# Kernel tuning notes

Hardware: AMD Instinct MI355X
Metric: run time of the kernel (lower is better)

Reference implementation:

```python
import jax, jax.numpy as jnp
import numpy as np
import math

B, N, DS, DP, DH, H, PQK, PV = 1, 384, 384, 128, 16, 12, 4, 8
PKV = PQK + PV
EPS = 1e-8
SOFTPLUS_INV_1 = 0.541324854612918


def setup_inputs() -> dict:
    key = jax.random.key(0)
    ks = jax.random.split(key, 20)
    W = lambda k, shp: (jax.random.normal(k, shp, dtype=jnp.float32) * 0.02)
    s = jax.random.normal(ks[0], (B, N, DS), dtype=jnp.float32)
    z = jax.random.normal(ks[1], (B, N, N, DP), dtype=jnp.float32)
    # random rigid frames: orthonormal rotations via QR + translations
    rot = jnp.linalg.qr(jax.random.normal(ks[2], (B, N, 3, 3), dtype=jnp.float32))[0]
    trans = jax.random.normal(ks[3], (B, N, 3), dtype=jnp.float32)
    square_mask = jnp.zeros((B, 1, N, N), dtype=jnp.float32)
    HC = H * DH
    COUT = H * (DP + DH + PV * 4)  # 2112
    return {
        "s": s, "z": z, "rot": rot, "trans": trans, "square_mask": square_mask,
        "Wq": W(ks[4], (DS, HC)), "bq": jnp.zeros((HC,), jnp.float32),
        "Wkv": W(ks[5], (DS, 2 * HC)), "bkv": jnp.zeros((2 * HC,), jnp.float32),
        "Wq_pts": W(ks[6], (DS, H * PQK * 3)), "bq_pts": jnp.zeros((H * PQK * 3,), jnp.float32),
        "Wkv_pts": W(ks[7], (DS, H * PKV * 3)), "bkv_pts": jnp.zeros((H * PKV * 3,), jnp.float32),
        "Wb": W(ks[8], (DP, H)), "bb": jnp.zeros((H,), jnp.float32),
        "head_weights": jnp.full((H,), SOFTPLUS_INV_1, dtype=jnp.float32),
        "Wout": W(ks[9], (COUT, DS)), "bout": jnp.zeros((DS,), jnp.float32),
    }


def _points(lin, rot, trans, npts):
    # lin: [B,N,3*H*npts] laid out as 3 coord-chunks of H*npts each (torch split+stack)
    pts = jnp.swapaxes(lin.reshape(B, N, 3, H * npts), -1, -2)  # [B,N,H*npts,3]
    pts = jnp.einsum('bnij,bnpj->bnpi', rot, pts) + trans[:, :, None, :]  # frame apply
    return pts.reshape(B, N, H, npts, 3)


def reference(s, z, rot, trans, square_mask, Wq, bq, Wkv, bkv, Wq_pts, bq_pts,
              Wkv_pts, bkv_pts, Wb, bb, head_weights, Wout, bout):
    q = (s @ Wq + bq).reshape(B, N, H, DH)
    kv = (s @ Wkv + bkv).reshape(B, N, H, 2 * DH)
    k, v = kv[..., :DH], kv[..., DH:]

    q_pts = _points(s @ Wq_pts + bq_pts, rot, trans, PQK)          # [B,N,H,PQK,3]
    kv_pts = _points(s @ Wkv_pts + bkv_pts, rot, trans, PKV)       # [B,N,H,PKV,3]
    k_pts, v_pts = kv_pts[..., :PQK, :], kv_pts[..., PQK:, :]

    bias = z @ Wb + bb                                             # [B,Nq,Nk,H]
    attn = jnp.einsum('bqhd,bkhd->bhqk', q, k) * math.sqrt(1.0 / (3 * DH))
    attn = attn + math.sqrt(1.0 / 3) * jnp.transpose(bias, (0, 3, 1, 2))

    diff = q_pts[:, :, None] - k_pts[:, None]                      # [B,Nq,Nk,H,PQK,3]
    dist2 = jnp.sum(diff * diff, axis=-1)                          # [B,Nq,Nk,H,PQK]
    hw = jax.nn.softplus(head_weights) * math.sqrt(1.0 / (3 * (PQK * 9.0 / 2)))
    pt_att = -0.5 * jnp.sum(dist2 * hw[None, None, None, :, None], axis=-1)  # [B,Nq,Nk,H]

    attn = attn + square_mask + jnp.transpose(pt_att, (0, 3, 1, 2))
    attn = jax.nn.softmax(attn, axis=-1)                           # [B,H,Nq,Nk]

    o = jnp.einsum('bhqk,bkhd->bqhd', attn, v).reshape(B, N, H * DH)
    o_pts = jnp.einsum('bhqk,bkhpc->bqhpc', attn, v_pts)           # [B,N,H,PV,3]
    # frame invert_apply: R^T (p - t)
    o_pts = jnp.einsum('bnji,bnhpj->bnhpi', rot, o_pts - trans[:, :, None, None, :])
    o_pts_norm = jnp.sqrt(jnp.sum(o_pts ** 2, axis=-1) + EPS).reshape(B, N, H * PV)
    o_pts_flat = o_pts.reshape(B, N, H * PV, 3)
    o_pair = jnp.einsum('bhqk,bqkc->bqhc', attn, z).reshape(B, N, H * DP)

    cat = jnp.concatenate(
        [o, o_pts_flat[..., 0], o_pts_flat[..., 1], o_pts_flat[..., 2], o_pts_norm, o_pair],
        axis=-1)
    return cat @ Wout + bout
```

## Files before the change

kernel.cpp:

```cpp
#include <hip/hip_runtime.h>
#include <math.h>

#define N     384
#define DSd   384
#define DP    128
#define DH    16
#define H     12
#define PQK   4
#define PV    8
#define HC    (H*DH)
#define PROJW 1152
#define NN    (N*N)
#define COUTD 2112
#define KSPL  4
#define KCH   96

__global__ __launch_bounds__(256) void pack_w(
    const float* __restrict__ Wq, const float* __restrict__ Wkv,
    const float* __restrict__ Wqp, const float* __restrict__ Wkvp,
    const float* __restrict__ bq, const float* __restrict__ bkv,
    const float* __restrict__ bqp, const float* __restrict__ bkvp,
    float* __restrict__ Wcat, float* __restrict__ bcat)
{
    const int i = blockIdx.x * 256 + threadIdx.x;
    if (i < DSd * PROJW) {
        const int r = i / PROJW, c = i % PROJW;
        float v;
        if (c < 192)      v = Wq[r*192 + c];
        else if (c < 576) v = Wkv[r*384 + (c-192)];
        else if (c < 720) v = Wqp[r*144 + (c-576)];
        else              v = Wkvp[r*432 + (c-720)];
        Wcat[i] = v;
    }
    if (i < PROJW) {
        float v;
        if (i < 192)      v = bq[i];
        else if (i < 576) v = bkv[i-192];
        else if (i < 720) v = bqp[i-576];
        else              v = bkvp[i-720];
        bcat[i] = v;
    }
}

__global__ __launch_bounds__(256) void gemm32x64(
    const float* __restrict__ A, const float* __restrict__ B,
    float* __restrict__ partial, int M, int Nc, int K, int kchunk)
{
    __shared__ float Ast[32][34];
    __shared__ float Bs[32][68];
    const int tid = threadIdx.x;
    const int tc = tid & 15, tr = tid >> 4;
    const int row0 = blockIdx.x * 32, col0 = blockIdx.y * 64;
    const int kbeg = blockIdx.z * kchunk;
    const int kend = kbeg + kchunk;
    float acc[2][4] = {};

    for (int kk = kbeg; kk < kend; kk += 32) {
        #pragma unroll
        for (int i = tid; i < 32*32; i += 256) {
            int r = i >> 5, c = i & 31;
            Ast[c][r] = A[(row0 + r) * K + kk + c];
        }
        #pragma unroll
        for (int i = tid; i < 32*64; i += 256) {
            int r = i >> 6, c = i & 63;
            Bs[r][c] = B[(kk + r) * Nc + col0 + c];
        }
        __syncthreads();
        #pragma unroll
        for (int p = 0; p < 32; ++p) {
            const float2 av = *(const float2*)&Ast[p][tr*2];
            const float4 bv = *(const float4*)&Bs[p][tc*4];
            acc[0][0] = fmaf(av.x, bv.x, acc[0][0]);
            acc[0][1] = fmaf(av.x, bv.y, acc[0][1]);
            acc[0][2] = fmaf(av.x, bv.z, acc[0][2]);
            acc[0][3] = fmaf(av.x, bv.w, acc[0][3]);
            acc[1][0] = fmaf(av.y, bv.x, acc[1][0]);
            acc[1][1] = fmaf(av.y, bv.y, acc[1][1]);
            acc[1][2] = fmaf(av.y, bv.z, acc[1][2]);
            acc[1][3] = fmaf(av.y, bv.w, acc[1][3]);
        }
        __syncthreads();
    }
    float* p0 = partial + ((size_t)blockIdx.z * M + row0 + tr*2) * Nc + col0 + tc*4;
    *(float4*)p0        = make_float4(acc[0][0], acc[0][1], acc[0][2], acc[0][3]);
    *(float4*)(p0 + Nc) = make_float4(acc[1][0], acc[1][1], acc[1][2], acc[1][3]);
}

__global__ __launch_bounds__(256) void reduce_kernel(
    const float* __restrict__ partial, const float* __restrict__ bias,
    float* __restrict__ out, int nc, int parts, int stride)
{
    const int i = blockIdx.x * 256 + threadIdx.x;
    float a = bias[i % nc];
    for (int t = 0; t < parts; ++t) a += partial[(size_t)t * stride + i];
    out[i] = a;
}

__global__ __launch_bounds__(192) void repack_kernel(
    const float* __restrict__ proj, const float* __restrict__ rot,
    const float* __restrict__ trans,
    float* __restrict__ q_t, float* __restrict__ k_t, float* __restrict__ vcat,
    float* __restrict__ qpts_t, float* __restrict__ kpts_t)
{
    const int n = blockIdx.x;
    const int tid = threadIdx.x;
    const float* pr = proj + n * PROJW;

    {
        int h = tid >> 4, d = tid & 15;
        q_t[(h*N + n)*DH + d]     = pr[h*DH + d];
        k_t[(h*N + n)*DH + d]     = pr[HC + h*2*DH + d];
        vcat[(h*40 + d)*N + n]    = pr[HC + h*2*DH + DH + d];
    }
    const float r00 = rot[n*9+0], r01 = rot[n*9+1], r02 = rot[n*9+2];
    const float r10 = rot[n*9+3], r11 = rot[n*9+4], r12 = rot[n*9+5];
    const float r20 = rot[n*9+6], r21 = rot[n*9+7], r22 = rot[n*9+8];
    const float t0 = trans[n*3+0], t1 = trans[n*3+1], t2 = trans[n*3+2];

    if (tid < H*PQK) {
        int p = tid;
        float l0 = pr[576 + 0*48 + p];
        float l1 = pr[576 + 1*48 + p];
        float l2 = pr[576 + 2*48 + p];
        int h = p / PQK, pt = p % PQK;
        float* dst = qpts_t + (h*N + n)*12 + pt*3;
        dst[0] = r00*l0 + r01*l1 + r02*l2 + t0;
        dst[1] = r10*l0 + r11*l1 + r12*l2 + t1;
        dst[2] = r20*l0 + r21*l1 + r22*l2 + t2;
    }
    if (tid < H*(PQK+PV)) {
        int p = tid;
        float l0 = pr[720 + 0*144 + p];
        float l1 = pr[720 + 1*144 + p];
        float l2 = pr[720 + 2*144 + p];
        int h = p / 12, pt = p % 12;
        float x0 = r00*l0 + r01*l1 + r02*l2 + t0;
        float x1 = r10*l0 + r11*l1 + r12*l2 + t1;
        float x2 = r20*l0 + r21*l1 + r22*l2 + t2;
        if (pt < PQK) {
            float* dst = kpts_t + (h*N + n)*12 + pt*3;
            dst[0] = x0; dst[1] = x1; dst[2] = x2;
        } else {
            const int j = 16 + (pt - PQK)*3;
            vcat[(h*40 + j+0)*N + n] = x0;
            vcat[(h*40 + j+1)*N + n] = x1;
            vcat[(h*40 + j+2)*N + n] = x2;
        }
    }
}

__global__ __launch_bounds__(256) void bias_kernel(
    const float* __restrict__ z, const float* __restrict__ Wb,
    const float* __restrict__ bb, float* __restrict__ biasattn)
{
    const int pair = blockIdx.x * 256 + threadIdx.x;
    const float4* zp = (const float4*)(z + (size_t)pair * DP);
    float acc[12] = {};
    #pragma unroll 4
    for (int c4 = 0; c4 < DP/4; ++c4) {
        const float4 zv = zp[c4];
        #pragma unroll
        for (int h = 0; h < H; ++h) {
            acc[h] = fmaf(zv.x, Wb[(c4*4+0)*H + h], acc[h]);
            acc[h] = fmaf(zv.y, Wb[(c4*4+1)*H + h], acc[h]);
            acc[h] = fmaf(zv.z, Wb[(c4*4+2)*H + h], acc[h]);
            acc[h] = fmaf(zv.w, Wb[(c4*4+3)*H + h], acc[h]);
        }
    }
    const float sc = 0.5773502691896258f;
    #pragma unroll
    for (int h = 0; h < H; ++h)
        biasattn[h*NN + pair] = (acc[h] + bb[h]) * sc;
}

__global__ __launch_bounds__(128) void attn_kernel(
    const float* __restrict__ q_t, const float* __restrict__ k_t,
    const float* __restrict__ qpts_t, const float* __restrict__ kpts_t,
    const float* __restrict__ mask, const float* __restrict__ head_weights,
    float* __restrict__ biasattn)
{
    const int h  = blockIdx.x % H;
    const int qi = blockIdx.x / H;
    const int tid = threadIdx.x;
    __shared__ float logits[N];
    __shared__ float red[4];

    const float4* qv = (const float4*)(q_t + (h*N + qi)*DH);
    const float4 q0 = qv[0], q1 = qv[1], q2 = qv[2], q3 = qv[3];
    const float4* qpv = (const float4*)(qpts_t + (h*N + qi)*12);
    const float4 p0 = qpv[0], p1 = qpv[1], p2 = qpv[2];
    const float hw = log1pf(expf(head_weights[h])) * 0.13608276348795434f;

    float lmax = -1e30f;
    for (int k = tid; k < N; k += 128) {
        const float4* kr = (const float4*)(k_t + (h*N + k)*DH);
        const float4 a0 = kr[0], a1 = kr[1], a2 = kr[2], a3 = kr[3];
        float dot = q0.x*a0.x;
        dot = fmaf(q0.y, a0.y, dot); dot = fmaf(q0.z, a0.z, dot); dot = fmaf(q0.w, a0.w, dot);
        dot = fmaf(q1.x, a1.x, dot); dot = fmaf(q1.y, a1.y, dot); dot = fmaf(q1.z, a1.z, dot); dot = fmaf(q1.w, a1.w, dot);
        dot = fmaf(q2.x, a2.x, dot); dot = fmaf(q2.y, a2.y, dot); dot = fmaf(q2.z, a2.z, dot); dot = fmaf(q2.w, a2.w, dot);
        dot = fmaf(q3.x, a3.x, dot); dot = fmaf(q3.y, a3.y, dot); dot = fmaf(q3.z, a3.z, dot); dot = fmaf(q3.w, a3.w, dot);
        const float4* kp = (const float4*)(kpts_t + (h*N + k)*12);
        const float4 b0 = kp[0], b1 = kp[1], b2 = kp[2];
        float df, d2;
        df = p0.x-b0.x; d2 = df*df;
        df = p0.y-b0.y; d2 = fmaf(df, df, d2);
        df = p0.z-b0.z; d2 = fmaf(df, df, d2);
        df = p0.w-b0.w; d2 = fmaf(df, df, d2);
        df = p1.x-b1.x; d2 = fmaf(df, df, d2);
        df = p1.y-b1.y; d2 = fmaf(df, df, d2);
        df = p1.z-b1.z; d2 = fmaf(df, df, d2);
        df = p1.w-b1.w; d2 = fmaf(df, df, d2);
        df = p2.x-b2.x; d2 = fmaf(df, df, d2);
        df = p2.y-b2.y; d2 = fmaf(df, df, d2);
        df = p2.z-b2.z; d2 = fmaf(df, df, d2);
        df = p2.w-b2.w; d2 = fmaf(df, df, d2);
        float l = fmaf(dot, 0.14433756729740643f,
                       biasattn[h*NN + qi*N + k] + mask[qi*N + k])
                - 0.5f * hw * d2;
        logits[k] = l;
        lmax = fmaxf(lmax, l);
    }
    #pragma unroll
    for (int o = 32; o > 0; o >>= 1) lmax = fmaxf(lmax, __shfl_xor(lmax, o));
    if ((tid & 63) == 0) red[tid >> 6] = lmax;
    __syncthreads();
    const float m = fmaxf(red[0], red[1]);
    float lsum = 0.f;
    for (int k = tid; k < N; k += 128) {
        float e = __expf(logits[k] - m);
        logits[k] = e;
        lsum += e;
    }
    #pragma unroll
    for (int o = 32; o > 0; o >>= 1) lsum += __shfl_xor(lsum, o);
    if ((tid & 63) == 0) red[2 + (tid >> 6)] = lsum;
    __syncthreads();
    const float inv = 1.f / (red[2] + red[3]);
    for (int k = tid; k < N; k += 128)
        biasattn[h*NN + qi*N + k] = logits[k] * inv;
}

__global__ __launch_bounds__(256) void opair_partial(
    const float* __restrict__ attn, const float* __restrict__ vcat,
    const float* __restrict__ z, float* __restrict__ P1, float* __restrict__ P2)
{
    const int qi = blockIdx.x, kq = blockIdx.y;
    const int k0 = kq * KCH;
    const int tid = threadIdx.x;
    __shared__ float pzs[2][H][DP];

    {
        const int c = tid & 127;
        const int half = __builtin_amdgcn_readfirstlane(tid >> 7);
        const float* zp = z + ((size_t)qi*N + k0 + half*48)*DP + c;
        const float* arow = attn + qi*N + k0 + half*48;
        float acc[12] = {};
        #pragma unroll 4
        for (int k = 0; k < 48; ++k) {
            const float zv = zp[(size_t)k*DP];
            #pragma unroll
            for (int h = 0; h < H; ++h)
                acc[h] = fmaf(arow[h*NN + k], zv, acc[h]);
        }
        #pragma unroll
        for (int h = 0; h < H; ++h) pzs[half][h][c] = acc[h];
    }
    {
        const int wv = __builtin_amdgcn_readfirstlane(tid >> 6);
        const int lane = tid & 63;
        if (lane < 40) {
            const int h0 = wv*3;
            const float* a0 = attn + (h0+0)*NN + qi*N + k0;
            const float* a1 = attn + (h0+1)*NN + qi*N + k0;
            const float* a2 = attn + (h0+2)*NN + qi*N + k0;
            const float* v0 = vcat + ((h0+0)*40 + lane)*N + k0;
            const float* v1 = vcat + ((h0+1)*40 + lane)*N + k0;
            const float* v2 = vcat + ((h0+2)*40 + lane)*N + k0;
            float s0 = 0.f, s1 = 0.f, s2 = 0.f;
            #pragma unroll 4
            for (int k = 0; k < KCH; ++k) {
                s0 = fmaf(a0[k], v0[k], s0);
                s1 = fmaf(a1[k], v1[k], s1);
                s2 = fmaf(a2[k], v2[k], s2);
            }
            float* pb = P1 + ((size_t)qi*KSPL + kq)*480;
            const int j0 = (lane < 16) ? (h0+0)*16 + lane : 192 + (h0+0)*24 + (lane-16);
            const int j1 = (lane < 16) ? (h0+1)*16 + lane : 192 + (h0+1)*24 + (lane-16);
            const int j2 = (lane < 16) ? (h0+2)*16 + lane : 192 + (h0+2)*24 + (lane-16);
            pb[j0] = s0; pb[j1] = s1; pb[j2] = s2;
        }
    }
    __syncthreads();
    for (int i = tid; i < H*DP; i += 256)
        P2[((size_t)qi*KSPL + kq)*(H*DP) + i] = pzs[0][i>>7][i&127] + pzs[1][i>>7][i&127];
}

__global__ __launch_bounds__(256) void combine_kernel(
    const float* __restrict__ P1, const float* __restrict__ P2,
    const float* __restrict__ rot, const float* __restrict__ trans,
    float* __restrict__ cat)
{
    const int qi = blockIdx.x;
    const int tid = threadIdx.x;
    __shared__ float catv[COUTD];
    __shared__ float praw[H*PV*3];

    for (int j = tid; j < 480; j += 256) {
        const float* p = P1 + (size_t)qi*KSPL*480 + j;
        float s = p[0] + p[480] + p[960] + p[1440];
        if (j < 192) catv[j] = s; else praw[j-192] = s;
    }
    for (int i = tid; i < H*DP; i += 256) {
        const float* p = P2 + (size_t)qi*KSPL*(H*DP) + i;
        catv[576 + i] = p[0] + p[1536] + p[3072] + p[4608];
    }
    __syncthreads();
    if (tid < H*PV) {
        const float* rr = rot + qi*9;
        const float t0 = trans[qi*3+0], t1 = trans[qi*3+1], t2 = trans[qi*3+2];
        float y0 = praw[tid*3+0] - t0;
        float y1 = praw[tid*3+1] - t1;
        float y2 = praw[tid*3+2] - t2;
        float f0 = rr[0]*y0 + rr[3]*y1 + rr[6]*y2;
        float f1 = rr[1]*y0 + rr[4]*y1 + rr[7]*y2;
        float f2 = rr[2]*y0 + rr[5]*y1 + rr[8]*y2;
        catv[HC + 0*96 + tid] = f0;
        catv[HC + 1*96 + tid] = f1;
        catv[HC + 2*96 + tid] = f2;
        catv[HC + 3*96 + tid] = sqrtf(f0*f0 + f1*f1 + f2*f2 + 1e-8f);
    }
    __syncthreads();
    float4* dst = (float4*)(cat + (size_t)qi * COUTD);
    const float4* src = (const float4*)catv;
    for (int i = tid; i < COUTD/4; i += 256) dst[i] = src[i];
}

extern "C" void kernel_launch(void* const* d_in, const int* in_sizes, int n_in,
                              void* d_out, int out_size, void* d_ws, size_t ws_size,
                              hipStream_t stream)
{
    const float* s       = (const float*)d_in[0];
    const float* z       = (const float*)d_in[1];
    const float* rot     = (const float*)d_in[2];
    const float* trans   = (const float*)d_in[3];
    const float* mask    = (const float*)d_in[4];
    const float* Wq      = (const float*)d_in[5];
    const float* bq      = (const float*)d_in[6];
    const float* Wkv     = (const float*)d_in[7];
    const float* bkv     = (const float*)d_in[8];
    const float* Wq_pts  = (const float*)d_in[9];
    const float* bq_pts  = (const float*)d_in[10];
    const float* Wkv_pts = (const float*)d_in[11];
    const float* bkv_pts = (const float*)d_in[12];
    const float* Wb      = (const float*)d_in[13];
    const float* bb      = (const float*)d_in[14];
    const float* hwts    = (const float*)d_in[15];
    const float* Wout    = (const float*)d_in[16];
    const float* bout    = (const float*)d_in[17];
    float* out = (float*)d_out;
    float* ws  = (float*)d_ws;

    float* ba     = ws;
    float* cat    = ba     + 1769472;
    float* q_t    = cat    + 811008;
    float* k_t    = q_t    + 73728;
    float* qpts_t = k_t    + 73728;
    float* kpts_t = qpts_t + 55296;
    float* vcat   = kpts_t + 55296;
    float* X      = vcat   + 184320;
    float* proj     = X;
    float* partialP = X + 442368;
    float* Wcat     = X + 1327104;
    float* bcat     = X + 1769472;
    float* P1       = X;
    float* P2       = X + 737280;
    float* partialF = X;

    pack_w<<<1728, 256, 0, stream>>>(Wq, Wkv, Wq_pts, Wkv_pts, bq, bkv, bq_pts, bkv_pts, Wcat, bcat);
    gemm32x64<<<dim3(12,18,2), 256, 0, stream>>>(s, Wcat, partialP, N, PROJW, DSd, 192);
    reduce_kernel<<<1728, 256, 0, stream>>>(partialP, bcat, proj, PROJW, 2, 442368);
    repack_kernel<<<N, 192, 0, stream>>>(proj, rot, trans, q_t, k_t, vcat, qpts_t, kpts_t);
    bias_kernel<<<NN/256, 256, 0, stream>>>(z, Wb, bb, ba);
    attn_kernel<<<N*H, 128, 0, stream>>>(q_t, k_t, qpts_t, kpts_t, mask, hwts, ba);
    opair_partial<<<dim3(N, KSPL), 256, 0, stream>>>(ba, vcat, z, P1, P2);
    combine_kernel<<<N, 256, 0, stream>>>(P1, P2, rot, trans, cat);
    gemm32x64<<<dim3(12,6,11), 256, 0, stream>>>(cat, Wout, partialF, N, 384, COUTD, 192);
    reduce_kernel<<<576, 256, 0, stream>>>(partialF, bout, out, 384, 11, NN);
}
```

Before: 319.4 us.

## Coalesce z reads in bias and pair-output kernels via LDS staging and float2 loads

The bias kernel now stages 64 rows of z into padded shared memory with coalesced loads. Each wave then computes 3 of the 12 heads, replacing the per-thread strided float4 reads of whole rows. The opair_partial kernel splits the key chunk across 4 waves, loads z as coalesced float2 into registers, and reduces four partial sums through larger shared memory, with a launch-bounds occupancy hint added. The aim is to cut uncoalesced global traffic on the large z tensor, at the cost of more shared memory, more register pressure from the 24-entry register tile, and 4x more bias blocks.

```diff
diff --git a/kernel.cpp b/kernel.cpp
--- a/kernel.cpp
+++ b/kernel.cpp
@@ -154,24 +154,28 @@
     const float* __restrict__ z, const float* __restrict__ Wb,
     const float* __restrict__ bb, float* __restrict__ biasattn)
 {
-    const int pair = blockIdx.x * 256 + threadIdx.x;
-    const float4* zp = (const float4*)(z + (size_t)pair * DP);
-    float acc[12] = {};
+    __shared__ float zt[64][DP+1];
+    const int tid = threadIdx.x;
+    const int base = blockIdx.x * 64;
+    for (int i = tid; i < 64*DP; i += 256)
+        zt[i >> 7][i & 127] = z[(size_t)base*DP + i];
+    __syncthreads();
+
+    const int p = tid & 63;
+    const int g3 = __builtin_amdgcn_readfirstlane((tid >> 6) * 3);
+    float a0 = 0.f, a1 = 0.f, a2 = 0.f;
     #pragma unroll 4
-    for (int c4 = 0; c4 < DP/4; ++c4) {
-        const float4 zv = zp[c4];
-        #pragma unroll
-        for (int h = 0; h < H; ++h) {
-            acc[h] = fmaf(zv.x, Wb[(c4*4+0)*H + h], acc[h]);
-            acc[h] = fmaf(zv.y, Wb[(c4*4+1)*H + h], acc[h]);
-            acc[h] = fmaf(zv.z, Wb[(c4*4+2)*H + h], acc[h]);
-            acc[h] = fmaf(zv.w, Wb[(c4*4+3)*H + h], acc[h]);
-        }
+    for (int c = 0; c < DP; ++c) {
+        float zv = zt[p][c];
+        a0 = fmaf(zv, Wb[c*H + g3 + 0], a0);
+        a1 = fmaf(zv, Wb[c*H + g3 + 1], a1);
+        a2 = fmaf(zv, Wb[c*H + g3 + 2], a2);
     }
     const float sc = 0.5773502691896258f;
-    #pragma unroll
-    for (int h = 0; h < H; ++h)
-        biasattn[h*NN + pair] = (acc[h] + bb[h]) * sc;
+    const int pair = base + p;
+    biasattn[(g3+0)*NN + pair] = (a0 + bb[g3+0]) * sc;
+    biasattn[(g3+1)*NN + pair] = (a1 + bb[g3+1]) * sc;
+    biasattn[(g3+2)*NN + pair] = (a2 + bb[g3+2]) * sc;
 }
 
 __global__ __launch_bounds__(128) void attn_kernel(
@@ -242,34 +246,42 @@
         biasattn[h*NN + qi*N + k] = logits[k] * inv;
 }
 
-__global__ __launch_bounds__(256) void opair_partial(
+__global__ __launch_bounds__(256, 4) void opair_partial(
     const float* __restrict__ attn, const float* __restrict__ vcat,
     const float* __restrict__ z, float* __restrict__ P1, float* __restrict__ P2)
 {
     const int qi = blockIdx.x, kq = blockIdx.y;
     const int k0 = kq * KCH;
     const int tid = threadIdx.x;
-    __shared__ float pzs[2][H][DP];
+    const int wv = __builtin_amdgcn_readfirstlane(tid >> 6);
+    const int lane = tid & 63;
+    __shared__ float pzs[4][H][DP];
 
     {
-        const int c = tid & 127;
-        const int half = __builtin_amdgcn_readfirstlane(tid >> 7);
-        const float* zp = z + ((size_t)qi*N + k0 + half*48)*DP + c;
-        const float* arow = attn + qi*N + k0 + half*48;
-        float acc[12] = {};
-        #pragma unroll 4
-        for (int k = 0; k < 48; ++k) {
-            const float zv = zp[(size_t)k*DP];
+        const int c2 = lane * 2;
+        const int kw0 = k0 + wv * 24;
+        const float* zp = z + ((size_t)qi*N + kw0)*DP + c2;
+        float2 zreg[24];
+        #pragma unroll
+        for (int k = 0; k < 24; ++k)
+            zreg[k] = *(const float2*)(zp + (size_t)k*DP);
+        float2 acc[12];
+        #pragma unroll
+        for (int h = 0; h < 12; ++h) acc[h] = make_float2(0.f, 0.f);
+        #pragma unroll
+        for (int h = 0; h < 12; ++h) {
+            const float* sa = attn + h*NN + qi*N + kw0;
             #pragma unroll
-            for (int h = 0; h < H; ++h)
-                acc[h] = fmaf(arow[h*NN + k], zv, acc[h]);
-        }
-        #pragma unroll
-        for (int h = 0; h < H; ++h) pzs[half][h][c] = acc[h];
+            for (int k = 0; k < 24; ++k) {
+                acc[h].x = fmaf(sa[k], zreg[k].x, acc[h].x);
+                acc[h].y = fmaf(sa[k], zreg[k].y, acc[h].y);
+            }
+        }
+        #pragma unroll
+        for (int h = 0; h < 12; ++h)
+            *(float2*)&pzs[wv][h][c2] = acc[h];
     }
     {
-        const int wv = __builtin_amdgcn_readfirstlane(tid >> 6);
-        const int lane = tid & 63;
         if (lane < 40) {
             const int h0 = wv*3;
             const float* a0 = attn + (h0+0)*NN + qi*N + k0;
@@ -293,8 +305,11 @@
         }
     }
     __syncthreads();
-    for (int i = tid; i < H*DP; i += 256)
-        P2[((size_t)qi*KSPL + kq)*(H*DP) + i] = pzs[0][i>>7][i&127] + pzs[1][i>>7][i&127];
+    for (int i = tid; i < H*DP; i += 256) {
+        const int h = i >> 7, c = i & 127;
+        P2[((size_t)qi*KSPL + kq)*(H*DP) + i] =
+            pzs[0][h][c] + pzs[1][h][c] + pzs[2][h][c] + pzs[3][h][c];
+    }
 }
 
 __global__ __launch_bounds__(256) void combine_kernel(
@@ -382,7 +397,7 @@
     gemm32x64<<<dim3(12,18,2), 256, 0, stream>>>(s, Wcat, partialP, N, PROJW, DSd, 192);
     reduce_kernel<<<1728, 256, 0, stream>>>(partialP, bcat, proj, PROJW, 2, 442368);
     repack_kernel<<<N, 192, 0, stream>>>(proj, rot, trans, q_t, k_t, vcat, qpts_t, kpts_t);
-    bias_kernel<<<NN/256, 256, 0, stream>>>(z, Wb, bb, ba);
+    bias_kernel<<<NN/64, 256, 0, stream>>>(z, Wb, bb, ba);
     attn_kernel<<<N*H, 128, 0, stream>>>(q_t, k_t, qpts_t, kpts_t, mask, hwts, ba);
     opair_partial<<<dim3(N, KSPL), 256, 0, stream>>>(ba, vcat, z, P1, P2);
     combine_kernel<<<N, 256, 0, stream>>>(P1, P2, rot, trans, cat);
```

Measured after the change: 321.3 us. Within noise of the previous version (+0.6%).
